# Kernel tuning notes

Measured on AMD Instinct MI355X. Metric: run time of the kernel, lower is better.

The kernel has to match this reference:

```python
import jax, jax.numpy as jnp
import numpy as np

N = 2048
HID = 1024
Z = 256
DIM = 128 + 64 * 3 + 32 * 5  # 480
FAN = 128 * 128 + 64 * 64 + 32 * 32  # total fan-in over all CG paths


def _ln(x, g, b, eps=1e-6):
    mu = jnp.mean(x, axis=-1, keepdims=True)
    var = jnp.mean((x - mu) ** 2, axis=-1, keepdims=True)
    return (x - mu) * jax.lax.rsqrt(var + eps) * g + b


def _fctp(t, w0, w1, w2):
    # FullyConnectedTensorProduct(irreps, irreps, 'HIDx0e'):
    # only l1==l2 -> 0e paths survive; CG is delta_{m1,m2}/sqrt(2l+1).
    x0 = t[:, :128]                       # 128x0e
    x1 = t[:, 128:320].reshape(-1, 64, 3)  # 64x1o
    x2 = t[:, 320:480].reshape(-1, 32, 5)  # 32x2e
    e0 = jnp.einsum('bu,bv,uvh->bh', x0, x0, w0)
    e1 = jnp.einsum('bum,bvm,uvh->bh', x1, x1, w1) / np.sqrt(3.0)
    e2 = jnp.einsum('bum,bvm,uvh->bh', x2, x2, w2) / np.sqrt(5.0)
    return (e0 + e1 + e2) / np.sqrt(float(FAN))  # component normalization


def _head(t, w0, w1, w2, W1, b1, g1, be1, W2, b2, g2, be2):
    h = _fctp(t, w0, w1, w2)
    h = jax.nn.silu(_ln(h @ W1 + b1, g1, be1))
    h = jax.nn.silu(_ln(h @ W2 + b2, g2, be2))
    return h  # [N, Z]


def setup_inputs() -> dict:
    key = jax.random.key(0)
    ks = jax.random.split(key, 6)
    return {
        'tensor_in': jax.random.normal(ks[0], (N, DIM), jnp.float32),
        'w0': jax.random.normal(ks[1], (128, 128, HID), jnp.float32),
        'w1': jax.random.normal(ks[2], (64, 64, HID), jnp.float32),
        'w2': jax.random.normal(ks[3], (32, 32, HID), jnp.float32),
        'W1': jax.random.normal(ks[4], (HID, HID), jnp.float32) / np.sqrt(HID),
        'b1': jnp.zeros((HID,), jnp.float32),
        'g1': jnp.ones((HID,), jnp.float32),
        'be1': jnp.zeros((HID,), jnp.float32),
        'W2': jax.random.normal(ks[5], (HID, Z), jnp.float32) / np.sqrt(HID),
        'b2': jnp.zeros((Z,), jnp.float32),
        'g2': jnp.ones((Z,), jnp.float32),
        'be2': jnp.zeros((Z,), jnp.float32),
    }


def reference(tensor_in, w0, w1, w2, W1, b1, g1, be1, W2, b2, g2, be2):
    f = lambda t: _head(t, w0, w1, w2, W1, b1, g1, be1, W2, b2, g2, be2)
    x, pullback = jax.vjp(f, tensor_in)
    # torch: grad(x, tensor_in, grad_outputs=ones_like(x), create_graph=True)
    y = pullback(jnp.ones_like(x))[0]
    return x, y
```

## Files before the change

kernel.cpp:

```cpp
#include <hip/hip_runtime.h>
#include <math.h>

typedef unsigned short u16;
typedef __bf16 bf16x8 __attribute__((ext_vector_type(8)));
typedef float f32x4 __attribute__((ext_vector_type(4)));

#define NPACK  11264
#define NVALID 10864
#define BASE1  8256
#define BASE2  10336

__device__ __forceinline__ u16 f2bf(float f) {
    unsigned u = __builtin_bit_cast(unsigned, f);
    u += 0x7FFFu + ((u >> 16) & 1u);
    return (u16)(u >> 16);
}
__device__ __forceinline__ float bf2f(u16 h) {
    return __builtin_bit_cast(float, ((unsigned)h) << 16);
}

#define GLOAD_LDS16(g, l)                                                     \
    __builtin_amdgcn_global_load_lds(                                         \
        (const __attribute__((address_space(1))) void*)(g),                   \
        (__attribute__((address_space(3))) void*)(l), 16, 0, 0)

__device__ __forceinline__ int pk0(int a, int b) {
    int u = min(a, b), v = max(a, b);
    return u * 128 - (u * (u - 1)) / 2 + (v - u);
}
__device__ __forceinline__ int pk1(int a, int b) {
    int u = min(a, b), v = max(a, b);
    return BASE1 + u * 64 - (u * (u - 1)) / 2 + (v - u);
}
__device__ __forceinline__ int pk2(int a, int b) {
    int u = min(a, b), v = max(a, b);
    return BASE2 + u * 32 - (u * (u - 1)) / 2 + (v - u);
}

__global__ __launch_bounds__(256) void k_uvall(u16* __restrict__ tab) {
    int j = blockIdx.x * 256 + threadIdx.x;
    if (j < 16384) {
        int u = j >> 7, v = j & 127;
        if (v >= u) tab[pk0(u, v)] = (u16)((u << 7) | v);
    } else if (j < 20480) {
        int k = j - 16384, u = k >> 6, v = k & 63;
        if (v >= u) tab[pk1(u, v)] = (u16)((1 << 14) | (u << 7) | v);
    } else if (j < 21504) {
        int k = j - 20480, u = k >> 5, v = k & 31;
        if (v >= u) tab[pk2(u, v)] = (u16)((2 << 14) | (u << 7) | v);
    } else {
        int k = j - 21504;
        if (NVALID + k < NPACK) tab[NVALID + k] = 0xFFFFu;
    }
}

__global__ __launch_bounds__(256) void k_packw(const float* __restrict__ w0,
                                               const float* __restrict__ w1,
                                               const float* __restrict__ w2,
                                               const u16* __restrict__ tab,
                                               u16* __restrict__ Wsym,
                                               u16* __restrict__ Wt) {
    __shared__ u16 tile[32][258];
    __shared__ u16 te[32];
    int i0 = blockIdx.x * 32, h0 = blockIdx.y * 256, tid = threadIdx.x;
    if (tid < 32) te[tid] = tab[i0 + tid];
    __syncthreads();
    const float s1 = 0.57735026918962576f, s2 = 0.44721359549995794f;
    for (int il = 0; il < 32; il++) {
        unsigned e = te[il];
        float val = 0.f;
        if ((e >> 14) != 3) {
            int seg = e >> 14, u = (e >> 7) & 127, v = e & 127;
            const float* wb; int S; float sc;
            if (seg == 0)      { wb = w0; S = 128; sc = 1.f; }
            else if (seg == 1) { wb = w1; S = 64;  sc = s1; }
            else               { wb = w2; S = 32;  sc = s2; }
            val = sc * (wb[(size_t)(u * S + v) * 1024 + h0 + tid] +
                        wb[(size_t)(v * S + u) * 1024 + h0 + tid]);
        }
        u16 bv = f2bf(val);
        Wsym[(size_t)(i0 + il) * 1024 + h0 + tid] = bv;
        tile[il][tid] = bv;
    }
    __syncthreads();
    union { u16 a[32]; uint4 q[4]; } pk;
#pragma unroll
    for (int il = 0; il < 32; il++) pk.a[il] = tile[il][tid];
    uint4* dst = (uint4*)(Wt + (size_t)(h0 + tid) * NPACK + i0);
#pragma unroll
    for (int q = 0; q < 4; q++) dst[q] = pk.q[q];
}

__global__ __launch_bounds__(256) void k_convert(const float* __restrict__ in,
                                                 u16* __restrict__ out, int n4) {
    int i = blockIdx.x * 256 + threadIdx.x;
    if (i >= n4) return;
    float4 v = ((const float4*)in)[i];
    union { u16 a[4]; unsigned long long q; } o;
    o.a[0] = f2bf(v.x); o.a[1] = f2bf(v.y); o.a[2] = f2bf(v.z); o.a[3] = f2bf(v.w);
    ((unsigned long long*)out)[i] = o.q;
}

__global__ __launch_bounds__(256) void k_transpose(const float* __restrict__ in, int R, int C,
                                                   u16* __restrict__ out, int ldOut) {
    __shared__ float tile[32][33];
    int tr0 = blockIdx.y * 32;
    int tc0 = blockIdx.x * 32;
    int lr = threadIdx.x >> 5;
    int lc = threadIdx.x & 31;
#pragma unroll
    for (int i = 0; i < 4; i++) {
        int rr = lr + i * 8;
        tile[rr][lc] = in[(size_t)(tr0 + rr) * C + tc0 + lc];
    }
    __syncthreads();
#pragma unroll
    for (int i = 0; i < 4; i++) {
        int rr = lr + i * 8;
        out[(size_t)(tc0 + rr) * ldOut + tr0 + lc] = f2bf(tile[lc][rr]);
    }
}

__global__ __launch_bounds__(256) void k_features_pack(const float* __restrict__ t,
                                                       const u16* __restrict__ tab,
                                                       u16* __restrict__ P) {
    __shared__ u16 tab_s[NPACK];
    __shared__ float tr[480];
    int b = blockIdx.x, tid = threadIdx.x;
    for (int j = tid; j < NPACK / 8; j += 256)
        ((uint4*)tab_s)[j] = ((const uint4*)tab)[j];
    for (int j = tid; j < 480; j += 256) tr[j] = t[(size_t)b * 480 + j];
    __syncthreads();
    u16* row = P + (size_t)b * NPACK;
    for (int i = tid; i < NPACK; i += 256) {
        unsigned e = tab_s[i];
        float p = 0.f;
        if ((e >> 14) != 3) {
            int seg = e >> 14, u = (e >> 7) & 127, v = e & 127;
            if (seg == 0) p = tr[u] * tr[v];
            else if (seg == 1) {
                const float* x1 = tr + 128;
                p = x1[u*3]*x1[v*3] + x1[u*3+1]*x1[v*3+1] + x1[u*3+2]*x1[v*3+2];
            } else {
                const float* x2 = tr + 320;
#pragma unroll
                for (int m = 0; m < 5; m++) p += x2[u*5+m] * x2[v*5+m];
            }
            if (u == v) p *= 0.5f;
        }
        row[i] = f2bf(p);
    }
}

__global__ __launch_bounds__(256) void k_gemm2(const u16* __restrict__ A, int ldA,
                                               const u16* __restrict__ B, int ldB,
                                               int kLen, float scale,
                                               const float* __restrict__ bias,
                                               float* __restrict__ Cf,
                                               u16* __restrict__ Cb, int ldC,
                                               float* __restrict__ Cpart, int Mtot,
                                               int swz) {
    __shared__ u16 As[2][128 * 32];
    __shared__ u16 Bs[2][128 * 32];
    const int tid = threadIdx.x;
    const int wave = tid >> 6, lane = tid & 63;
    const int wm = wave >> 1, wn = wave & 1;
    int nT, mT, z;
    if (swz == 1) {
        int L = blockIdx.x;
        z = L & 7; int r = L >> 3;
        nT = r >> 4; mT = r & 15;
    } else if (swz == 2) {
        int L = blockIdx.x;
        int c = L & 7, r = L >> 3;
        nT = (r % 11) * 8 + c; mT = r / 11; z = 0;
    } else {
        nT = blockIdx.x; mT = blockIdx.y; z = blockIdx.z;
    }
    const int m0 = mT * 128, n0 = nT * 128;
    const size_t kOff = (size_t)z * kLen;

    const int chl = (((lane & 3) ^ ((lane >> 3) & 3))) * 8;
    const u16* aG = A + (size_t)(m0 + wave * 32 + (lane >> 2)) * ldA + kOff + chl;
    const u16* bG = B + (size_t)(n0 + wave * 32 + (lane >> 2)) * ldB + kOff + chl;
    const size_t aS = (size_t)16 * ldA;
    const size_t bS = (size_t)16 * ldB;
    u16* aL0 = &As[0][(wave * 32) * 32];
    u16* aL1 = &As[0][(wave * 32 + 16) * 32];
    u16* aH0 = &As[1][(wave * 32) * 32];
    u16* aH1 = &As[1][(wave * 32 + 16) * 32];
    u16* bL0 = &Bs[0][(wave * 32) * 32];
    u16* bL1 = &Bs[0][(wave * 32 + 16) * 32];
    u16* bH0 = &Bs[1][(wave * 32) * 32];
    u16* bH1 = &Bs[1][(wave * 32 + 16) * 32];

    f32x4 acc[4][4];
#pragma unroll
    for (int i = 0; i < 4; i++)
#pragma unroll
        for (int j = 0; j < 4; j++) acc[i][j] = (f32x4){0.f, 0.f, 0.f, 0.f};

    const int ml = lane & 15, kq8 = lane >> 4;
    const int kqs = (kq8 ^ ((ml >> 1) & 3)) * 8;
    const u16* aRd0 = &As[0][(wm * 64 + ml) * 32 + kqs];
    const u16* bRd0 = &Bs[0][(wn * 64 + ml) * 32 + kqs];
    const u16* aRd1 = &As[1][(wm * 64 + ml) * 32 + kqs];
    const u16* bRd1 = &Bs[1][(wn * 64 + ml) * 32 + kqs];

    for (int k = 0; k < kLen; k += 64) {
        GLOAD_LDS16(aG, aL0);
        GLOAD_LDS16(aG + aS, aL1);
        GLOAD_LDS16(aG + 32, aH0);
        GLOAD_LDS16(aG + aS + 32, aH1);
        GLOAD_LDS16(bG, bL0);
        GLOAD_LDS16(bG + bS, bL1);
        GLOAD_LDS16(bG + 32, bH0);
        GLOAD_LDS16(bG + bS + 32, bH1);
        aG += 64; bG += 64;
        __syncthreads();
        {
            bf16x8 af[4], bfv[4];
#pragma unroll
            for (int i = 0; i < 4; i++) af[i]  = *(const bf16x8*)(aRd0 + i * 16 * 32);
#pragma unroll
            for (int j = 0; j < 4; j++) bfv[j] = *(const bf16x8*)(bRd0 + j * 16 * 32);
#pragma unroll
            for (int i = 0; i < 4; i++)
#pragma unroll
                for (int j = 0; j < 4; j++)
                    acc[i][j] = __builtin_amdgcn_mfma_f32_16x16x32_bf16(af[i], bfv[j], acc[i][j], 0, 0, 0);
        }
        {
            bf16x8 af[4], bfv[4];
#pragma unroll
            for (int i = 0; i < 4; i++) af[i]  = *(const bf16x8*)(aRd1 + i * 16 * 32);
#pragma unroll
            for (int j = 0; j < 4; j++) bfv[j] = *(const bf16x8*)(bRd1 + j * 16 * 32);
#pragma unroll
            for (int i = 0; i < 4; i++)
#pragma unroll
                for (int j = 0; j < 4; j++)
                    acc[i][j] = __builtin_amdgcn_mfma_f32_16x16x32_bf16(af[i], bfv[j], acc[i][j], 0, 0, 0);
        }
        __syncthreads();
    }

    const int q = lane >> 4, nl = lane & 15;
    if (Cpart) {
        float* outP = Cpart + (size_t)z * Mtot * ldC;
#pragma unroll
        for (int i = 0; i < 4; i++)
#pragma unroll
            for (int j = 0; j < 4; j++)
#pragma unroll
                for (int reg = 0; reg < 4; reg++) {
                    int row = m0 + wm * 64 + i * 16 + q * 4 + reg;
                    int col = n0 + wn * 64 + j * 16 + nl;
                    outP[(size_t)row * ldC + col] = acc[i][j][reg];
                }
    } else {
#pragma unroll
        for (int i = 0; i < 4; i++)
#pragma unroll
            for (int j = 0; j < 4; j++)
#pragma unroll
                for (int reg = 0; reg < 4; reg++) {
                    int row = m0 + wm * 64 + i * 16 + q * 4 + reg;
                    int col = n0 + wn * 64 + j * 16 + nl;
                    float v = acc[i][j][reg] * scale + (bias ? bias[col] : 0.0f);
                    if (Cf) Cf[(size_t)row * ldC + col] = v;
                    else    Cb[(size_t)row * ldC + col] = f2bf(v);
                }
    }
}

__global__ __launch_bounds__(256) void k_reduce(const float* __restrict__ part, size_t stride,
                                                int SK, int total, int N, float scale,
                                                const float* __restrict__ bias,
                                                float* __restrict__ outF, u16* __restrict__ outB) {
    int i = blockIdx.x * 256 + threadIdx.x;
    if (i >= total) return;
    float s = 0.f;
    for (int z = 0; z < SK; z++) s += part[(size_t)z * stride + i];
    float v = s * scale + (bias ? bias[i % N] : 0.0f);
    if (outF) outF[i] = v;
    else      outB[i] = f2bf(v);
}

__device__ __forceinline__ float blockReduce(float v, float* red) {
#pragma unroll
    for (int off = 32; off > 0; off >>= 1) v += __shfl_down(v, off);
    __syncthreads();
    if ((threadIdx.x & 63) == 0) red[threadIdx.x >> 6] = v;
    __syncthreads();
    return red[0] + red[1] + red[2] + red[3];
}

__global__ __launch_bounds__(256) void k_ln_fwd(const float* __restrict__ X, int D,
    const float* __restrict__ g, const float* __restrict__ be,
    float* __restrict__ mu_out, float* __restrict__ r_out,
    u16* __restrict__ a_bf, float* __restrict__ a_f32) {
    __shared__ float red[4];
    int b = blockIdx.x, tid = threadIdx.x;
    const float* x = X + (size_t)b * D;
    int nd = D >> 8;
    float s = 0.f, s2 = 0.f;
    for (int r = 0; r < nd; r++) { float v = x[tid + (r << 8)]; s += v; s2 += v * v; }
    s = blockReduce(s, red);
    s2 = blockReduce(s2, red);
    float mu = s / D;
    float var = s2 / D - mu * mu;
    float rst = rsqrtf(var + 1e-6f);
    if (tid == 0) { mu_out[b] = mu; r_out[b] = rst; }
    for (int r = 0; r < nd; r++) {
        int i = tid + (r << 8);
        float xh = (x[i] - mu) * rst;
        float ln = xh * g[i] + be[i];
        float a = ln / (1.0f + expf(-ln));
        if (a_bf)  a_bf[(size_t)b * D + i] = f2bf(a);
        if (a_f32) a_f32[(size_t)b * D + i] = a;
    }
}

__global__ __launch_bounds__(256) void k_ln_bwd(const float* __restrict__ dup,
    const float* __restrict__ X, const float* __restrict__ mu_in, const float* __restrict__ r_in,
    const float* __restrict__ g, const float* __restrict__ be,
    u16* __restrict__ out_bf, int D) {
    __shared__ float red[4];
    int b = blockIdx.x, tid = threadIdx.x;
    const float* x = X + (size_t)b * D;
    float mu = mu_in[b], rst = r_in[b];
    int nd = D >> 8;
    float w_[4], xh_[4];
    float sw = 0.f, swx = 0.f;
    for (int r = 0; r < nd; r++) {
        int i = tid + (r << 8);
        float xh = (x[i] - mu) * rst;
        float ln = xh * g[i] + be[i];
        float sg = 1.0f / (1.0f + expf(-ln));
        float dsilu = sg * (1.0f + ln * (1.0f - sg));
        float d = dup ? dup[(size_t)b * D + i] : 1.0f;
        float w = g[i] * dsilu * d;
        w_[r] = w; xh_[r] = xh;
        sw += w; swx += w * xh;
    }
    sw = blockReduce(sw, red);
    swx = blockReduce(swx, red);
    float invD = 1.0f / D;
    for (int r = 0; r < nd; r++) {
        int i = tid + (r << 8);
        float dx = rst * (w_[r] - sw * invD - xh_[r] * swx * invD);
        out_bf[(size_t)b * D + i] = f2bf(dx);
    }
}

__global__ __launch_bounds__(256) void k_contract_p(const u16* __restrict__ Gp,
                                                    const float* __restrict__ t,
                                                    float* __restrict__ y) {
    __shared__ u16 gp_s[NPACK];
    __shared__ float xs[480];
    int b = blockIdx.x, tid = threadIdx.x;
    const uint4* gsrc = (const uint4*)(Gp + (size_t)b * NPACK);
    for (int j = tid; j < NPACK / 8; j += 256) ((uint4*)gp_s)[j] = gsrc[j];
    for (int j = tid; j < 480; j += 256) xs[j] = t[(size_t)b * 480 + j];
    __syncthreads();
    int wave = tid >> 6, lane = tid & 63;
    float* yr = y + (size_t)b * 480;
    for (int r = 0; r < 32; r++) {
        int u = wave * 32 + r;
        int v0 = lane, v1 = lane + 64;
        float s = bf2f(gp_s[pk0(u, v0)]) * xs[v0] + bf2f(gp_s[pk0(u, v1)]) * xs[v1];
#pragma unroll
        for (int off = 32; off > 0; off >>= 1) s += __shfl_down(s, off);
        if (lane == 0) yr[u] = s;
    }
    for (int r = 0; r < 16; r++) {
        int u = wave * 16 + r;
        float gv = bf2f(gp_s[pk1(u, lane)]);
        float a0 = gv * xs[128 + lane * 3 + 0];
        float a1 = gv * xs[128 + lane * 3 + 1];
        float a2 = gv * xs[128 + lane * 3 + 2];
#pragma unroll
        for (int off = 32; off > 0; off >>= 1) {
            a0 += __shfl_down(a0, off);
            a1 += __shfl_down(a1, off);
            a2 += __shfl_down(a2, off);
        }
        if (lane == 0) {
            yr[128 + u * 3 + 0] = a0;
            yr[128 + u * 3 + 1] = a1;
            yr[128 + u * 3 + 2] = a2;
        }
    }
    for (int r = 0; r < 8; r++) {
        int u = wave * 8 + r;
        bool act = lane < 32;
        float gv = act ? bf2f(gp_s[pk2(u, act ? lane : 0)]) : 0.f;
        float a[5];
#pragma unroll
        for (int m = 0; m < 5; m++)
            a[m] = act ? gv * xs[320 + lane * 5 + m] : 0.f;
#pragma unroll
        for (int off = 32; off > 0; off >>= 1)
#pragma unroll
            for (int m = 0; m < 5; m++) a[m] += __shfl_down(a[m], off);
        if (lane == 0)
#pragma unroll
            for (int m = 0; m < 5; m++) yr[320 + u * 5 + m] = a[m];
    }
}

extern "C" void kernel_launch(void* const* d_in, const int* in_sizes, int n_in,
                              void* d_out, int out_size, void* d_ws, size_t ws_size,
                              hipStream_t stream) {
    const float* t   = (const float*)d_in[0];
    const float* w0  = (const float*)d_in[1];
    const float* w1  = (const float*)d_in[2];
    const float* w2  = (const float*)d_in[3];
    const float* W1  = (const float*)d_in[4];
    const float* b1  = (const float*)d_in[5];
    const float* g1  = (const float*)d_in[6];
    const float* be1 = (const float*)d_in[7];
    const float* W2  = (const float*)d_in[8];
    const float* b2  = (const float*)d_in[9];
    const float* g2  = (const float*)d_in[10];
    const float* be2 = (const float*)d_in[11];

    float* xout = (float*)d_out;
    float* yout = xout + (size_t)2048 * 256;

    char* ws = (char*)d_ws;
    size_t off = 0;
    auto alloc = [&](size_t bytes) -> void* {
        void* p = ws + off;
        off += (bytes + 255) & ~(size_t)255;
        return p;
    };
    u16*   PG    = (u16*)alloc((size_t)2048 * NPACK * 2);
    u16*   Wsym  = (u16*)alloc((size_t)NPACK * 1024 * 2);
    u16*   Wt    = (u16*)alloc((size_t)1024 * NPACK * 2);
    u16*   uvtab = (u16*)alloc((size_t)NPACK * 2);
    u16*   W1b   = (u16*)alloc((size_t)1024 * 1024 * 2);
    u16*   W1tb  = (u16*)alloc((size_t)1024 * 1024 * 2);
    u16*   W2b   = (u16*)alloc((size_t)1024 * 256 * 2);
    u16*   W2tb  = (u16*)alloc((size_t)256 * 1024 * 2);
    u16*   h_bf  = (u16*)alloc((size_t)2048 * 1024 * 2);
    float* h1pre = (float*)alloc((size_t)2048 * 1024 * 4);
    float* mu1   = (float*)alloc(2048 * 4);
    float* r1    = (float*)alloc(2048 * 4);
    u16*   a1_bf = (u16*)alloc((size_t)2048 * 1024 * 2);
    float* h2pre = (float*)alloc((size_t)2048 * 256 * 4);
    float* mu2   = (float*)alloc(2048 * 4);
    float* r2    = (float*)alloc(2048 * 4);
    u16*   dh2b  = (u16*)alloc((size_t)2048 * 256 * 2);
    float* d_a1  = (float*)alloc((size_t)2048 * 1024 * 4);
    u16*   dh1b  = (u16*)alloc((size_t)2048 * 1024 * 2);
    u16*   de_bf = (u16*)alloc((size_t)2048 * 1024 * 2);
    float* Cpart = (float*)(ws + off);
    size_t cpartBytes = (ws_size > off) ? (ws_size - off) : 0;
    (void)in_sizes; (void)n_in; (void)out_size;

    const float sF = 1.0f / sqrtf(21504.0f);

    auto gemm = [&](const u16* A, int ldA, const u16* B, int ldB, int M, int N, int K,
                    int SKwant, float scale, const float* bias,
                    float* Cf, u16* Cb, int ldC) {
        int SK = SKwant;
        size_t slice = (size_t)M * ldC * 4;
        if (SK > 1 && cpartBytes < 2 * slice) SK = 1;
        if (SK > 1 && (size_t)SK * slice > cpartBytes) SK = (int)(cpartBytes / slice);
        while (SK > 1 && !((K % SK) == 0 && ((K / SK) % 64) == 0)) SK--;
        dim3 grid(N / 128, M / 128, SK);
        if (SK > 1) {
            k_gemm2<<<grid, 256, 0, stream>>>(A, ldA, B, ldB, K / SK, 0.f, nullptr,
                                              nullptr, nullptr, ldC, Cpart, M, 0);
            int total = M * ldC;
            k_reduce<<<(total + 255) / 256, 256, 0, stream>>>(Cpart, (size_t)M * ldC, SK,
                                                              total, N, scale, bias, Cf, Cb);
        } else {
            k_gemm2<<<grid, 256, 0, stream>>>(A, ldA, B, ldB, K, scale, bias,
                                              Cf, Cb, ldC, nullptr, M, 0);
        }
    };

    k_uvall<<<(21504 + NPACK - NVALID + 255) / 256, 256, 0, stream>>>(uvtab);
    k_packw<<<dim3(NPACK / 32, 4), 256, 0, stream>>>(w0, w1, w2, uvtab, Wsym, Wt);

    k_transpose<<<dim3(32, 32), 256, 0, stream>>>(W1, 1024, 1024, W1tb, 1024);
    k_transpose<<<dim3(8, 32), 256, 0, stream>>>(W2, 1024, 256, W2tb, 1024);
    k_convert<<<1024 * 1024 / 1024, 256, 0, stream>>>(W1, W1b, 1024 * 1024 / 4);
    k_convert<<<1024 * 256 / 1024, 256, 0, stream>>>(W2, W2b, 1024 * 256 / 4);

    k_features_pack<<<2048, 256, 0, stream>>>(t, uvtab, PG);

    k_gemm2<<<dim3(1024), 256, 0, stream>>>(PG, NPACK, Wt, NPACK, NPACK / 8, 0.f, nullptr,
                                            nullptr, nullptr, 1024, Cpart, 2048, 1);
    {
        int total = 2048 * 1024;
        k_reduce<<<(total + 255) / 256, 256, 0, stream>>>(Cpart, (size_t)2048 * 1024, 8,
                                                          total, 1024, sF, nullptr,
                                                          nullptr, h_bf);
    }

    gemm(h_bf, 1024, W1tb, 1024, 2048, 1024, 1024, 4, 1.0f, b1, h1pre, nullptr, 1024);
    k_ln_fwd<<<2048, 256, 0, stream>>>(h1pre, 1024, g1, be1, mu1, r1, a1_bf, nullptr);
    gemm(a1_bf, 1024, W2tb, 1024, 2048, 256, 1024, 8, 1.0f, b2, h2pre, nullptr, 256);
    k_ln_fwd<<<2048, 256, 0, stream>>>(h2pre, 256, g2, be2, mu2, r2, nullptr, xout);

    k_ln_bwd<<<2048, 256, 0, stream>>>(nullptr, h2pre, mu2, r2, g2, be2, dh2b, 256);
    gemm(dh2b, 256, W2b, 256, 2048, 1024, 256, 4, 1.0f, nullptr, d_a1, nullptr, 1024);
    k_ln_bwd<<<2048, 256, 0, stream>>>(d_a1, h1pre, mu1, r1, g1, be1, dh1b, 1024);
    gemm(dh1b, 1024, W1b, 1024, 2048, 1024, 1024, 4, sF, nullptr, nullptr, de_bf, 1024);

    u16* Gp = PG;
    k_gemm2<<<dim3(1408), 256, 0, stream>>>(de_bf, 1024, Wsym, 1024, 1024, 1.0f, nullptr,
                                            nullptr, Gp, NPACK, nullptr, 2048, 2);

    k_contract_p<<<2048, 256, 0, stream>>>(Gp, t, yout);
}
```

Measured before the change: 517.1 us.

## Double-buffer GEMM K-loop so global-to-LDS loads overlap MFMA compute

Splits the K=64 step into two K=32 halves stored in the two LDS buffers and software-pipelines them. The next half is staged via global_load_lds while MFMAs run on the current half, and there is one barrier per 32-wide step instead of loading everything and then waiting. This is meant to hide global memory latency behind compute. It adds more barriers per unit of K, and its correctness depends on the barrier ordering when the buffers are reused.

Result: slower. 552.7 us (+6.9%).

```diff
diff --git a/kernel.cpp b/kernel.cpp
--- a/kernel.cpp
+++ b/kernel.cpp
@@ -185,14 +185,14 @@
     const u16* bG = B + (size_t)(n0 + wave * 32 + (lane >> 2)) * ldB + kOff + chl;
     const size_t aS = (size_t)16 * ldA;
     const size_t bS = (size_t)16 * ldB;
-    u16* aL0 = &As[0][(wave * 32) * 32];
-    u16* aL1 = &As[0][(wave * 32 + 16) * 32];
-    u16* aH0 = &As[1][(wave * 32) * 32];
-    u16* aH1 = &As[1][(wave * 32 + 16) * 32];
-    u16* bL0 = &Bs[0][(wave * 32) * 32];
-    u16* bL1 = &Bs[0][(wave * 32 + 16) * 32];
-    u16* bH0 = &Bs[1][(wave * 32) * 32];
-    u16* bH1 = &Bs[1][(wave * 32 + 16) * 32];
+    u16* const aW0  = &As[0][(wave * 32) * 32];
+    u16* const aW0b = &As[0][(wave * 32 + 16) * 32];
+    u16* const aW1  = &As[1][(wave * 32) * 32];
+    u16* const aW1b = &As[1][(wave * 32 + 16) * 32];
+    u16* const bW0  = &Bs[0][(wave * 32) * 32];
+    u16* const bW0b = &Bs[0][(wave * 32 + 16) * 32];
+    u16* const bW1  = &Bs[1][(wave * 32) * 32];
+    u16* const bW1b = &Bs[1][(wave * 32 + 16) * 32];
 
     f32x4 acc[4][4];
 #pragma unroll
@@ -207,42 +207,46 @@
     const u16* aRd1 = &As[1][(wm * 64 + ml) * 32 + kqs];
     const u16* bRd1 = &Bs[1][(wn * 64 + ml) * 32 + kqs];
 
-    for (int k = 0; k < kLen; k += 64) {
-        GLOAD_LDS16(aG, aL0);
-        GLOAD_LDS16(aG + aS, aL1);
-        GLOAD_LDS16(aG + 32, aH0);
-        GLOAD_LDS16(aG + aS + 32, aH1);
-        GLOAD_LDS16(bG, bL0);
-        GLOAD_LDS16(bG + bS, bL1);
-        GLOAD_LDS16(bG + 32, bH0);
-        GLOAD_LDS16(bG + bS + 32, bH1);
-        aG += 64; bG += 64;
+    auto stage = [&](u16* a0, u16* a1, u16* b0, u16* b1) {
+        GLOAD_LDS16(aG, a0);
+        GLOAD_LDS16(aG + aS, a1);
+        GLOAD_LDS16(bG, b0);
+        GLOAD_LDS16(bG + bS, b1);
+        aG += 32; bG += 32;
+    };
+    auto compute = [&](const u16* aRdP, const u16* bRdP) {
+        bf16x8 af[4], bfv[4];
+#pragma unroll
+        for (int i = 0; i < 4; i++) af[i]  = *(const bf16x8*)(aRdP + i * 16 * 32);
+#pragma unroll
+        for (int j = 0; j < 4; j++) bfv[j] = *(const bf16x8*)(bRdP + j * 16 * 32);
+#pragma unroll
+        for (int i = 0; i < 4; i++)
+#pragma unroll
+            for (int j = 0; j < 4; j++)
+                acc[i][j] = __builtin_amdgcn_mfma_f32_16x16x32_bf16(af[i], bfv[j], acc[i][j], 0, 0, 0);
+    };
+
+    const int last = (kLen >> 5) - 1;
+    stage(aW0, aW0b, bW0, bW0b);
+    __syncthreads();
+    int t = 0;
+    while (t + 1 < last) {
+        stage(aW1, aW1b, bW1, bW1b);
+        compute(aRd0, bRd0);
         __syncthreads();
-        {
-            bf16x8 af[4], bfv[4];
-#pragma unroll
-            for (int i = 0; i < 4; i++) af[i]  = *(const bf16x8*)(aRd0 + i * 16 * 32);
-#pragma unroll
-            for (int j = 0; j < 4; j++) bfv[j] = *(const bf16x8*)(bRd0 + j * 16 * 32);
-#pragma unroll
-            for (int i = 0; i < 4; i++)
-#pragma unroll
-                for (int j = 0; j < 4; j++)
-                    acc[i][j] = __builtin_amdgcn_mfma_f32_16x16x32_bf16(af[i], bfv[j], acc[i][j], 0, 0, 0);
-        }
-        {
-            bf16x8 af[4], bfv[4];
-#pragma unroll
-            for (int i = 0; i < 4; i++) af[i]  = *(const bf16x8*)(aRd1 + i * 16 * 32);
-#pragma unroll
-            for (int j = 0; j < 4; j++) bfv[j] = *(const bf16x8*)(bRd1 + j * 16 * 32);
-#pragma unroll
-            for (int i = 0; i < 4; i++)
-#pragma unroll
-                for (int j = 0; j < 4; j++)
-                    acc[i][j] = __builtin_amdgcn_mfma_f32_16x16x32_bf16(af[i], bfv[j], acc[i][j], 0, 0, 0);
-        }
+        stage(aW0, aW0b, bW0, bW0b);
+        compute(aRd1, bRd1);
         __syncthreads();
+        t += 2;
+    }
+    if (t < last) {
+        stage(aW1, aW1b, bW1, bW1b);
+        compute(aRd0, bRd0);
+        __syncthreads();
+        compute(aRd1, bRd1);
+    } else {
+        compute(aRd0, bRd0);
     }
 
     const int q = lane >> 4, nl = lane & 15;
```

## Add 256x256-tile 8-wave pipelined GEMM for the two large packed-feature GEMMs

Applied to the files above, without the earlier changes.

Adds a new GEMM kernel with 256x256 output tiles, 512 threads, and double-buffered LDS staging through direct global-to-LDS loads. It uses fine-grained vmcnt waits, barriers and setprio to interleave MFMA compute with loads. The kernel replaces the 128-tile GEMM in both the forward split-K feature GEMM and the backward Gp GEMM. Larger tiles raise arithmetic intensity and cut global traffic, but give fewer blocks (256 and 352) and higher register and LDS use per block.

New measurement: 530.8 us. 1.03x slower.

```diff
diff --git a/kernel.cpp b/kernel.cpp
--- a/kernel.cpp
+++ b/kernel.cpp
@@ -270,6 +270,136 @@
                     float v = acc[i][j][reg] * scale + (bias ? bias[col] : 0.0f);
                     if (Cf) Cf[(size_t)row * ldC + col] = v;
                     else    Cb[(size_t)row * ldC + col] = f2bf(v);
+                }
+    }
+}
+
+#define VMCNT8 asm volatile("s_waitcnt vmcnt(8)" ::: "memory")
+#define VMCNT4 asm volatile("s_waitcnt vmcnt(4)" ::: "memory")
+#define VMCNT0 asm volatile("s_waitcnt vmcnt(0)" ::: "memory")
+#define BARX() __builtin_amdgcn_s_barrier()
+
+#define STG_A(p, kh, rh, kb) GLOAD_LDS16(aB + (size_t)(rh) * aH + (kb) + (kh) * 32, \
+                                         &As[p][kh][((rh) * 128 + wave * 16) * 32])
+#define STG_B(p, kh, rh, kb) GLOAD_LDS16(bB + (size_t)(rh) * bH + (kb) + (kh) * 32, \
+                                         &Bs[p][kh][((rh) * 128 + wave * 16) * 32])
+#define RD_A8(p, kh) do { _Pragma("unroll") \
+    for (int f = 0; f < 8; f++) a[f] = *(const bf16x8*)&As[p][kh][aro + f * 512]; } while (0)
+#define RD_B2(p, kh, gg) do { \
+    b[(gg)]     = *(const bf16x8*)&Bs[p][kh][bro + (gg) * 512]; \
+    b[(gg) + 1] = *(const bf16x8*)&Bs[p][kh][bro + ((gg) + 1) * 512]; } while (0)
+#define MM2(cg) do { _Pragma("unroll") \
+    for (int f = 0; f < 8; f++) { \
+        acc[f][2*(cg)]   = __builtin_amdgcn_mfma_f32_16x16x32_bf16(a[f], b[2*(cg)],   acc[f][2*(cg)],   0, 0, 0); \
+        acc[f][2*(cg)+1] = __builtin_amdgcn_mfma_f32_16x16x32_bf16(a[f], b[2*(cg)+1], acc[f][2*(cg)+1], 0, 0, 0); } } while (0)
+
+__global__ __launch_bounds__(512, 2) void k_gemm256(const u16* __restrict__ A, int ldA,
+                                                    const u16* __restrict__ B, int ldB,
+                                                    int kLen, float scale,
+                                                    const float* __restrict__ bias,
+                                                    u16* __restrict__ Cb, int ldC,
+                                                    float* __restrict__ Cpart, int Mtot,
+                                                    int swz) {
+    __shared__ __align__(16) u16 As[2][2][256 * 32];
+    __shared__ __align__(16) u16 Bs[2][2][256 * 32];
+    const int tid = threadIdx.x;
+    const int lane = tid & 63, wave = tid >> 6;
+    const int wm = wave >> 2, wn = wave & 3;
+    int mT, nT, z;
+    if (swz == 1) { z = blockIdx.x & 7; int r = blockIdx.x >> 3; mT = r & 7; nT = r >> 3; }
+    else          { mT = blockIdx.x & 7; nT = blockIdx.x >> 3; z = 0; }
+    const int m0 = mT * 256, n0 = nT * 256;
+    const size_t kOff = (size_t)z * kLen;
+    const int nTi = kLen >> 6;
+
+    const int chl = ((tid & 3) ^ ((tid >> 3) & 3)) * 8;
+    const u16* aB = A + (size_t)(m0 + (tid >> 2)) * ldA + kOff + chl;
+    const u16* bB = B + (size_t)(n0 + (tid >> 2)) * ldB + kOff + chl;
+    const size_t aH = (size_t)128 * ldA;
+    const size_t bH = (size_t)128 * ldB;
+
+    const int ml = lane & 15, kq8 = lane >> 4;
+    const int kqs = (kq8 ^ ((ml >> 1) & 3)) * 8;
+    const int aro = (wm * 128 + ml) * 32 + kqs;
+    const int bro = (wn * 64 + ml) * 32 + kqs;
+
+    f32x4 acc[8][4];
+#pragma unroll
+    for (int f = 0; f < 8; f++)
+#pragma unroll
+        for (int g = 0; g < 4; g++) acc[f][g] = (f32x4){0.f, 0.f, 0.f, 0.f};
+    bf16x8 a[8], b[4];
+
+    STG_A(0, 0, 0, 0); STG_A(0, 0, 1, 0); STG_B(0, 0, 0, 0); STG_B(0, 0, 1, 0);
+    STG_A(0, 1, 0, 0); STG_A(0, 1, 1, 0); STG_B(0, 1, 0, 0); STG_B(0, 1, 1, 0);
+    if (nTi > 1) { STG_A(1, 0, 0, 64); STG_A(1, 0, 1, 64); STG_B(1, 0, 0, 64); STG_B(1, 0, 1, 64); }
+    VMCNT8;
+    BARX();
+
+    for (int t = 0; t < nTi; t++) {
+        const int p = t & 1, p1 = p ^ 1;
+        const int kb1 = (t + 1) << 6, kb2 = (t + 2) << 6;
+        const bool s1 = (t + 1) < nTi, s2 = (t + 2) < nTi, s3 = (t + 3) < nTi;
+        RD_A8(p, 0); RD_B2(p, 0, 0);
+        if (s1) { STG_A(p1, 1, 0, kb1); STG_A(p1, 1, 1, kb1); }
+        BARX();
+        __builtin_amdgcn_s_setprio(1);
+        MM2(0);
+        __builtin_amdgcn_s_setprio(0);
+        BARX();
+        RD_B2(p, 0, 2);
+        if (s1) { STG_B(p1, 1, 0, kb1); STG_B(p1, 1, 1, kb1); }
+        BARX();
+        __builtin_amdgcn_s_setprio(1);
+        MM2(1);
+        __builtin_amdgcn_s_setprio(0);
+        if (s2)      { VMCNT8; }
+        else if (s1) { VMCNT4; }
+        else         { VMCNT0; }
+        BARX();
+        RD_A8(p, 1); RD_B2(p, 1, 0);
+        if (s2) { STG_A(p, 0, 0, kb2); STG_A(p, 0, 1, kb2); }
+        BARX();
+        __builtin_amdgcn_s_setprio(1);
+        MM2(0);
+        __builtin_amdgcn_s_setprio(0);
+        BARX();
+        RD_B2(p, 1, 2);
+        if (s2) { STG_B(p, 0, 0, kb2); STG_B(p, 0, 1, kb2); }
+        BARX();
+        __builtin_amdgcn_s_setprio(1);
+        MM2(1);
+        __builtin_amdgcn_s_setprio(0);
+        if (s3)      { VMCNT8; }
+        else if (s2) { VMCNT4; }
+        else if (s1) { VMCNT0; }
+        BARX();
+    }
+
+    const int q = lane >> 4, nl = lane & 15;
+    if (Cpart) {
+        float* outP = Cpart + (size_t)z * Mtot * ldC;
+#pragma unroll
+        for (int f = 0; f < 8; f++)
+#pragma unroll
+            for (int g = 0; g < 4; g++)
+#pragma unroll
+                for (int reg = 0; reg < 4; reg++) {
+                    int row = m0 + wm * 128 + f * 16 + q * 4 + reg;
+                    int col = n0 + wn * 64 + g * 16 + nl;
+                    outP[(size_t)row * ldC + col] = acc[f][g][reg];
+                }
+    } else {
+#pragma unroll
+        for (int f = 0; f < 8; f++)
+#pragma unroll
+            for (int g = 0; g < 4; g++)
+#pragma unroll
+                for (int reg = 0; reg < 4; reg++) {
+                    int row = m0 + wm * 128 + f * 16 + q * 4 + reg;
+                    int col = n0 + wn * 64 + g * 16 + nl;
+                    float v = acc[f][g][reg] * scale + (bias ? bias[col] : 0.0f);
+                    Cb[(size_t)row * ldC + col] = f2bf(v);
                 }
     }
 }
@@ -493,8 +623,8 @@
 
     k_features_pack<<<2048, 256, 0, stream>>>(t, uvtab, PG);
 
-    k_gemm2<<<dim3(1024), 256, 0, stream>>>(PG, NPACK, Wt, NPACK, NPACK / 8, 0.f, nullptr,
-                                            nullptr, nullptr, 1024, Cpart, 2048, 1);
+    k_gemm256<<<dim3(256), 512, 0, stream>>>(PG, NPACK, Wt, NPACK, NPACK / 8, 0.f, nullptr,
+                                             nullptr, 1024, Cpart, 2048, 1);
     {
         int total = 2048 * 1024;
         k_reduce<<<(total + 255) / 256, 256, 0, stream>>>(Cpart, (size_t)2048 * 1024, 8,
@@ -513,8 +643,8 @@
     gemm(dh1b, 1024, W1b, 1024, 2048, 1024, 1024, 4, sF, nullptr, nullptr, de_bf, 1024);
 
     u16* Gp = PG;
-    k_gemm2<<<dim3(1408), 256, 0, stream>>>(de_bf, 1024, Wsym, 1024, 1024, 1.0f, nullptr,
-                                            nullptr, Gp, NPACK, nullptr, 2048, 2);
+    k_gemm256<<<dim3(352), 512, 0, stream>>>(de_bf, 1024, Wsym, 1024, 1024, 1.0f, nullptr,
+                                             Gp, NPACK, nullptr, 2048, 2);
 
     k_contract_p<<<2048, 256, 0, stream>>>(Gp, t, yout);
 }
```
